# Optimization experiments

Hardware: AMD Instinct MI355X
Metric: run time of the kernel (lower is better)

The kernel has to match this reference:

```python
import jax, jax.numpy as jnp
import numpy as np

IN, HID, RANK, B = 2048, 2048, 512, 8192


def setup_inputs() -> dict:
    key = jax.random.key(0)
    ks = jax.random.split(key, 16)
    s_in = 1.0 / np.sqrt(IN + HID)
    s_r = 1.0 / np.sqrt(RANK)
    inp = {
        "x": jax.random.normal(ks[0], (B, IN), jnp.float32),
        "h": jax.random.normal(ks[1], (B, HID), jnp.float32),
        "c": jax.random.normal(ks[2], (B, HID), jnp.float32),
    }
    names = ["i", "f", "c", "o"]
    for idx, g in enumerate(names):
        inp[f"U{g}"] = jax.random.uniform(ks[3 + 3 * idx], (IN + HID, RANK), jnp.float32, -s_in, s_in)
        inp[f"V{g}"] = jax.random.uniform(ks[4 + 3 * idx], (RANK, HID), jnp.float32, -s_r, s_r)
        inp[f"b{g}"] = jnp.zeros((HID,), jnp.float32)
    return inp


def reference(x, h, c, Ui, Vi, bi, Uf, Vf, bf, Uc, Vc, bc, Uo, Vo, bo):
    combined = jnp.concatenate([x, h], axis=1)  # [B, IN+HID]

    def gate(U, V, b):
        return (combined @ U) @ V + b  # low-rank: [B,R] then [B,HID]

    i = jax.nn.sigmoid(gate(Ui, Vi, bi))
    f = jax.nn.sigmoid(gate(Uf, Vf, bf))
    o = jax.nn.sigmoid(gate(Uo, Vo, bo))
    c_hat = jnp.tanh(gate(Uc, Vc, bc))
    c_new = f * c + i * c_hat
    h_new = o * jnp.tanh(c_new)
    return (h_new, c_new)
```

## Files before the change

kernel.cpp:

```cpp
#include <hip/hip_runtime.h>
#include <hip/hip_bf16.h>
#include <cstdint>
#include <cstddef>

typedef __bf16 bf16;
typedef __bf16 bf16x8 __attribute__((ext_vector_type(8)));
typedef float f32x4 __attribute__((ext_vector_type(4)));

#define BATCH 8192
#define IN_DIM 2048
#define HID 2048
#define RANK 512
#define KDIM 4096
#define NG 2048
#define CHUNK_ROWS 4096


__device__ __forceinline__ void gload16(const void* g, void* l) {
  __builtin_amdgcn_global_load_lds(
      (const __attribute__((address_space(1))) unsigned int*)g,
      (__attribute__((address_space(3))) unsigned int*)l, 16, 0, 0);
}

__device__ __forceinline__ float sigmoidf_(float x) {
  return 1.0f / (1.0f + __expf(-x));
}
__device__ __forceinline__ float tanhf_(float x) {
  return 1.0f - 2.0f / (__expf(2.0f * x) + 1.0f);
}

__device__ __forceinline__ void stage_half(const bf16* __restrict__ g0, int ld,
                                           int row0, int kcol, bf16* lbase, int tid) {
  const int wid = tid >> 6;
  #pragma unroll
  for (int q = 0; q < 2; ++q) {
    const int slot = q * 512 + tid;
    const int row = slot >> 3, cb = slot & 7;
    const int gcb = cb ^ (row & 7);
    gload16(g0 + (size_t)(row0 + row) * ld + kcol + gcb * 8,
            lbase + (size_t)(q * 64 + wid * 8) * 64);
  }
}

#define GBAR  __builtin_amdgcn_s_barrier()
#define LGKM0 asm volatile("s_waitcnt lgkmcnt(0)" ::: "memory")
#define VMC4  asm volatile("s_waitcnt vmcnt(4)" ::: "memory")
#define VMC8  asm volatile("s_waitcnt vmcnt(8)" ::: "memory")
#define SB0   __builtin_amdgcn_sched_barrier(0)

#define LD_Ap(PA, Q)                                                          \
  _Pragma("unroll") for (int ai = 0; ai < 2; ++ai)                            \
  _Pragma("unroll") for (int ks = 0; ks < 2; ++ks)                            \
    a[ai][ks] = *(const bf16x8*)((PA) + (wm + (Q) * 32 + ai * 16 + lr) * 64   \
                                 + ((((ks << 2) | lk) ^ sw) << 3));

#define LD_Bp(PB)                                                             \
  _Pragma("unroll") for (int j = 0; j < 4; ++j)                               \
  _Pragma("unroll") for (int ks = 0; ks < 2; ++ks)                            \
    b[j][ks] = *(const bf16x8*)((PB) + (wn + j * 16 + lr) * 64                \
                                 + ((((ks << 2) | lk) ^ sw) << 3));

#define MFMAQ(Q)                                                              \
  _Pragma("unroll") for (int ai = 0; ai < 2; ++ai)                            \
  _Pragma("unroll") for (int ks = 0; ks < 2; ++ks)                            \
  _Pragma("unroll") for (int j = 0; j < 4; ++j)                               \
    acc[(Q) * 2 + ai][j] = __builtin_amdgcn_mfma_f32_16x16x32_bf16(           \
        a[ai][ks], b[j][ks], acc[(Q) * 2 + ai][j], 0, 0, 0);

#define PHASE3(TOP, STAGE, Q, PFOP, TAILVM) \
  {                                         \
    TOP;                                    \
    STAGE;                                  \
    GBAR;                                   \
    LGKM0;                                  \
    __builtin_amdgcn_s_setprio(1);          \
    MFMAQ(Q);                               \
    __builtin_amdgcn_s_setprio(0);          \
    PFOP;                                   \
    SB0;                                    \
    TAILVM;                                 \
    GBAR;                                   \
  }

template <int NT>
__device__ __forceinline__ void gemm_core(const bf16* __restrict__ A, int lda, int m0,
                                          const bf16* __restrict__ B, int ldb, int n0,
                                          bf16* lds, f32x4 (&acc)[8][4]) {
  const int tid = threadIdx.x;
  const int wid = tid >> 6, lane = tid & 63;
  const int wm = (wid >> 2) * 128, wn = (wid & 3) * 64;
  const int lr = lane & 15, lk = lane >> 4;
  const int sw = lr & 7;
  bf16x8 a[2][2], b[4][2];

  bf16* Ab0 = lds;
  bf16* Ab1 = lds + 16384;
  bf16* Rg0 = lds + 2 * 16384;
  bf16* Rg1 = lds + 3 * 16384;
  bf16* Rg2 = lds + 4 * 16384;

  #pragma unroll
  for (int i = 0; i < 8; ++i)
    #pragma unroll
    for (int j = 0; j < 4; ++j) acc[i][j] = (f32x4){0.f, 0.f, 0.f, 0.f};

  stage_half(A, lda, m0,       0,   Ab0,        tid);
  stage_half(A, lda, m0 + 128, 0,   Ab0 + 8192, tid);
  stage_half(B, ldb, n0,       0,   Rg0,        tid);
  stage_half(B, ldb, n0 + 128, 0,   Rg0 + 8192, tid);
  stage_half(B, ldb, n0,       64,  Rg1,        tid);
  stage_half(B, ldb, n0 + 128, 64,  Rg1 + 8192, tid);
  stage_half(B, ldb, n0,       128, Rg2,        tid);
  stage_half(B, ldb, n0 + 128, 128, Rg2 + 8192, tid);
  VMC8;
  GBAR;
  LD_Bp(Rg0);

  bf16 *pBc = Rg0, *pBn = Rg1, *pBn2 = Rg2;
  bf16 *pAc = Ab0, *pAa = Ab1;
  for (int c = 0; c < NT; ++c) {
    const int kc1 = ((c + 1) & (NT - 1)) * 64;
    const int kc3 = ((c + 3) & (NT - 1)) * 64;
    PHASE3(LD_Ap(pAc, 0), stage_half(A, lda, m0,       kc1, pAa,        tid), 0,
           LD_Ap(pAc, 1), (void)0);
    PHASE3((void)0,       stage_half(A, lda, m0 + 128, kc1, pAa + 8192, tid), 1,
           LD_Ap(pAc, 2), (void)0);
    PHASE3((void)0,       stage_half(B, ldb, n0,       kc3, pBc,        tid), 2,
           LD_Ap(pAc, 3), (void)0);
    PHASE3((void)0,       stage_half(B, ldb, n0 + 128, kc3, pBc + 8192, tid), 3,
           LD_Bp(pBn),    VMC4);
    bf16* tt = pBc; pBc = pBn; pBn = pBn2; pBn2 = tt;
    tt = pAc; pAc = pAa; pAa = tt;
  }
}


__global__ void k_convert_combined(const float* __restrict__ x,
                                   const float* __restrict__ h,
                                   bf16* __restrict__ out) {
  size_t i4 = (size_t)blockIdx.x * blockDim.x + threadIdx.x;
  size_t base = i4 * 4;
  int col = (int)(base & (KDIM - 1));
  size_t row = base >> 12;
  const float* src = (col < IN_DIM) ? (x + row * IN_DIM + col)
                                    : (h + row * (size_t)HID + (col - IN_DIM));
  float4 v = *(const float4*)src;
  union { bf16 b[4]; uint2 u; } p;
  p.b[0] = (bf16)v.x; p.b[1] = (bf16)v.y; p.b[2] = (bf16)v.z; p.b[3] = (bf16)v.w;
  *(uint2*)(out + base) = p.u;
}


__global__ void k_tconv4(const float* __restrict__ s0, const float* __restrict__ s1,
                         const float* __restrict__ s2, const float* __restrict__ s3,
                         bf16* __restrict__ out, int nrow, int ncol,
                         long ostride, long gstride) {
  __shared__ float t[32][33];
  const float* in = blockIdx.z == 0 ? s0 : blockIdx.z == 1 ? s1
                  : blockIdx.z == 2 ? s2 : s3;
  bf16* o = out + (size_t)blockIdx.z * gstride;
  int c0 = blockIdx.x * 32, r0 = blockIdx.y * 32;
  int tx = threadIdx.x, ty = threadIdx.y;
  #pragma unroll
  for (int yy = ty; yy < 32; yy += 8)
    t[yy][tx] = in[(size_t)(r0 + yy) * ncol + c0 + tx];
  __syncthreads();
  #pragma unroll
  for (int yy = ty; yy < 32; yy += 8)
    o[(size_t)(c0 + yy) * ostride + r0 + tx] = (bf16)t[tx][yy];
}


__launch_bounds__(512, 2)
__global__ void k_gemm1(const bf16* __restrict__ A,
                        const bf16* __restrict__ Bt,
                        bf16* __restrict__ R) {
  __shared__ __align__(16) bf16 lds[81920];
  const int bx = blockIdx.x;
  const int id = (bx & 7) * 32 + (bx >> 3);
  const int m0 = (id >> 3) * 256, n0 = (id & 7) * 256;
  f32x4 acc[8][4];
  gemm_core<KDIM / 64>(A, KDIM, m0, Bt, KDIM, n0, lds, acc);

  const int tid = threadIdx.x;
  const int wid = tid >> 6, lane = tid & 63;
  const int wm = (wid >> 2) * 128, wn = (wid & 3) * 64;
  const int lr = lane & 15, lk = lane >> 4;
  #pragma unroll
  for (int i = 0; i < 8; ++i)
    #pragma unroll
    for (int j = 0; j < 4; ++j)
      #pragma unroll
      for (int v = 0; v < 4; ++v)
        R[(size_t)(m0 + wm + i * 16 + lk * 4 + v) * NG + (n0 + wn + j * 16 + lr)] =
            (bf16)acc[i][j][v];
}


__launch_bounds__(512, 2)
__global__ void k_gates(const bf16* __restrict__ Rb,
                        const bf16* __restrict__ Vt,
                        const float* __restrict__ b0, const float* __restrict__ b1,
                        const float* __restrict__ b2, const float* __restrict__ b3,
                        bf16* __restrict__ G, int m_base) {
  __shared__ __align__(16) bf16 lds[81920];
  const int bx = blockIdx.x;
  const int id = (bx & 7) * 64 + (bx >> 3);
  const int gate = id >> 7;
  const int mo = ((id >> 3) & 15) * 256;
  const int n0 = (id & 7) * 256;
  f32x4 acc[8][4];
  gemm_core<RANK / 64>(Rb + gate * RANK, NG, m_base + mo,
                       Vt + (size_t)gate * HID * RANK, RANK, n0, lds, acc);

  const int tid = threadIdx.x;
  const int wid = tid >> 6, lane = tid & 63;
  const int wm = (wid >> 2) * 128, wn = (wid & 3) * 64;
  const int lr = lane & 15, lk = lane >> 4;
  const float* bias = gate == 0 ? b0 : gate == 1 ? b1 : gate == 2 ? b2 : b3;
  const bool is_tanh = (gate == 2);
  bf16* Gg = G + (size_t)gate * CHUNK_ROWS * HID;
  #pragma unroll
  for (int j = 0; j < 4; ++j) {
    const int col = n0 + wn + j * 16 + lr;
    const float bj = bias[col];
    #pragma unroll
    for (int i = 0; i < 8; ++i)
      #pragma unroll
      for (int v = 0; v < 4; ++v) {
        const int row = mo + wm + i * 16 + lk * 4 + v;
        float p = acc[i][j][v] + bj;
        float av = is_tanh ? tanhf_(p) : sigmoidf_(p);
        Gg[(size_t)row * HID + col] = (bf16)av;
      }
  }
}


__global__ void k_ew(const bf16* __restrict__ G,
                     const float* __restrict__ cin,
                     float* __restrict__ hout, float* __restrict__ cout,
                     int m_base) {
  const size_t CHUNK = (size_t)CHUNK_ROWS * HID;
  const bf16* Gi = G;
  const bf16* Gf = G + CHUNK;
  const bf16* Gc = G + 2 * CHUNK;
  const bf16* Go = G + 3 * CHUNK;
  const size_t n8 = CHUNK / 8;
  for (size_t t = (size_t)blockIdx.x * blockDim.x + threadIdx.x; t < n8;
       t += (size_t)gridDim.x * blockDim.x) {
    size_t e = t * 8;
    bf16x8 vi = *(const bf16x8*)(Gi + e);
    bf16x8 vf = *(const bf16x8*)(Gf + e);
    bf16x8 vc = *(const bf16x8*)(Gc + e);
    bf16x8 vo = *(const bf16x8*)(Go + e);
    size_t ge = (size_t)m_base * HID + e;
    float4 c0 = *(const float4*)(cin + ge);
    float4 c1 = *(const float4*)(cin + ge + 4);
    float cc[8] = {c0.x, c0.y, c0.z, c0.w, c1.x, c1.y, c1.z, c1.w};
    float cn[8], hn[8];
    #pragma unroll
    for (int v = 0; v < 8; ++v) {
      float iv = (float)vi[v], fv = (float)vf[v], cv = (float)vc[v], ov = (float)vo[v];
      cn[v] = fv * cc[v] + iv * cv;
      hn[v] = ov * tanhf_(cn[v]);
    }
    *(float4*)(cout + ge)     = (float4){cn[0], cn[1], cn[2], cn[3]};
    *(float4*)(cout + ge + 4) = (float4){cn[4], cn[5], cn[6], cn[7]};
    *(float4*)(hout + ge)     = (float4){hn[0], hn[1], hn[2], hn[3]};
    *(float4*)(hout + ge + 4) = (float4){hn[4], hn[5], hn[6], hn[7]};
  }
}


extern "C" void kernel_launch(void* const* d_in, const int* in_sizes, int n_in,
                              void* d_out, int out_size, void* d_ws, size_t ws_size,
                              hipStream_t stream) {
  const float* x = (const float*)d_in[0];
  const float* h = (const float*)d_in[1];
  const float* c = (const float*)d_in[2];
  const float* U[4] = {(const float*)d_in[3], (const float*)d_in[6],
                       (const float*)d_in[9], (const float*)d_in[12]};
  const float* V[4] = {(const float*)d_in[4], (const float*)d_in[7],
                       (const float*)d_in[10], (const float*)d_in[13]};
  const float* b[4] = {(const float*)d_in[5], (const float*)d_in[8],
                       (const float*)d_in[11], (const float*)d_in[14]};

  char* ws = (char*)d_ws;
  bf16* combined = (bf16*)ws;
  bf16* Ut       = (bf16*)(ws + 67108864);
  bf16* Vt       = (bf16*)(ws + 67108864 + 16777216);
  bf16* Rbuf     = (bf16*)(ws + 67108864 + 16777216 + 8388608);
  bf16* G        = (bf16*)ws;

  float* hout = (float*)d_out;
  float* cout = hout + (size_t)BATCH * HID;

  k_convert_combined<<<(BATCH * (size_t)KDIM / 4) / 256, 256, 0, stream>>>(x, h, combined);

  k_tconv4<<<dim3(RANK / 32, KDIM / 32, 4), dim3(32, 8), 0, stream>>>(
      U[0], U[1], U[2], U[3], Ut, KDIM, RANK, KDIM, (long)RANK * KDIM);
  k_tconv4<<<dim3(HID / 32, RANK / 32, 4), dim3(32, 8), 0, stream>>>(
      V[0], V[1], V[2], V[3], Vt, RANK, HID, RANK, (long)HID * RANK);

  k_gemm1<<<256, 512, 0, stream>>>(combined, Ut, Rbuf);

  for (int chunk = 0; chunk < 2; ++chunk) {
    int m_base = chunk * CHUNK_ROWS;
    k_gates<<<512, 512, 0, stream>>>(Rbuf, Vt, b[0], b[1], b[2], b[3], G, m_base);
    k_ew<<<2048, 256, 0, stream>>>(G, c, hout, cout, m_base);
  }
}
```

Baseline: 346.7 us.

## Fuse four gate GEMMs with LSTM elementwise update in one kernel

Replaces the chunked gate GEMM plus elementwise kernels with a single kernel in which each block computes all four gate GEMMs for its output tile in sequence. Gate results are combined in registers (i*c_hat, then the c update, then h), so the bf16 gate intermediates are never written to or read back from global memory, and launches drop from four to one. In exchange, grid size falls from 512 to 256 blocks, register pressure rises from the extra 128-float state array, and the cin/cout/hout accesses become strided scalar loads and stores from the MFMA layout instead of vectorized ones.

```diff
diff --git a/kernel.cpp b/kernel.cpp
--- a/kernel.cpp
+++ b/kernel.cpp
@@ -13,7 +13,6 @@
 #define RANK 512
 #define KDIM 4096
 #define NG 2048
-#define CHUNK_ROWS 4096
 
 
 __device__ __forceinline__ void gload16(const void* g, void* l) {
@@ -44,6 +43,7 @@
 
 #define GBAR  __builtin_amdgcn_s_barrier()
 #define LGKM0 asm volatile("s_waitcnt lgkmcnt(0)" ::: "memory")
+#define VMC0  asm volatile("s_waitcnt vmcnt(0)" ::: "memory")
 #define VMC4  asm volatile("s_waitcnt vmcnt(4)" ::: "memory")
 #define VMC8  asm volatile("s_waitcnt vmcnt(8)" ::: "memory")
 #define SB0   __builtin_amdgcn_sched_barrier(0)
@@ -198,77 +198,58 @@
 
 
 __launch_bounds__(512, 2)
-__global__ void k_gates(const bf16* __restrict__ Rb,
+__global__ void k_fused(const bf16* __restrict__ Rb,
                         const bf16* __restrict__ Vt,
-                        const float* __restrict__ b0, const float* __restrict__ b1,
-                        const float* __restrict__ b2, const float* __restrict__ b3,
-                        bf16* __restrict__ G, int m_base) {
+                        const float* __restrict__ bi, const float* __restrict__ bf_,
+                        const float* __restrict__ bc, const float* __restrict__ bo,
+                        const float* __restrict__ cin,
+                        float* __restrict__ hout, float* __restrict__ cout) {
   __shared__ __align__(16) bf16 lds[81920];
   const int bx = blockIdx.x;
-  const int id = (bx & 7) * 64 + (bx >> 3);
-  const int gate = id >> 7;
-  const int mo = ((id >> 3) & 15) * 256;
-  const int n0 = (id & 7) * 256;
-  f32x4 acc[8][4];
-  gemm_core<RANK / 64>(Rb + gate * RANK, NG, m_base + mo,
-                       Vt + (size_t)gate * HID * RANK, RANK, n0, lds, acc);
-
+  const int id = (bx & 7) * 32 + (bx >> 3);
+  const int m0 = (id >> 3) * 256, n0 = (id & 7) * 256;
   const int tid = threadIdx.x;
   const int wid = tid >> 6, lane = tid & 63;
   const int wm = (wid >> 2) * 128, wn = (wid & 3) * 64;
   const int lr = lane & 15, lk = lane >> 4;
-  const float* bias = gate == 0 ? b0 : gate == 1 ? b1 : gate == 2 ? b2 : b3;
-  const bool is_tanh = (gate == 2);
-  bf16* Gg = G + (size_t)gate * CHUNK_ROWS * HID;
-  #pragma unroll
-  for (int j = 0; j < 4; ++j) {
-    const int col = n0 + wn + j * 16 + lr;
-    const float bj = bias[col];
+
+  f32x4 acc[8][4];
+  float sv[8][4][4];
+
+  #pragma unroll 1
+  for (int gi = 0; gi < 4; ++gi) {
+    const int g = ((gi & 1) << 1) | (gi >> 1);
+    if (gi) {
+      VMC0;
+      GBAR;
+    }
+    gemm_core<RANK / 64>(Rb + g * RANK, NG, m0,
+                         Vt + (size_t)g * HID * RANK, RANK, n0, lds, acc);
+    const float* bias = g == 0 ? bi : g == 1 ? bf_ : g == 2 ? bc : bo;
     #pragma unroll
-    for (int i = 0; i < 8; ++i)
+    for (int j = 0; j < 4; ++j) {
+      const int col = n0 + wn + j * 16 + lr;
+      const float bj = bias[col];
       #pragma unroll
-      for (int v = 0; v < 4; ++v) {
-        const int row = mo + wm + i * 16 + lk * 4 + v;
-        float p = acc[i][j][v] + bj;
-        float av = is_tanh ? tanhf_(p) : sigmoidf_(p);
-        Gg[(size_t)row * HID + col] = (bf16)av;
-      }
-  }
-}
-
-
-__global__ void k_ew(const bf16* __restrict__ G,
-                     const float* __restrict__ cin,
-                     float* __restrict__ hout, float* __restrict__ cout,
-                     int m_base) {
-  const size_t CHUNK = (size_t)CHUNK_ROWS * HID;
-  const bf16* Gi = G;
-  const bf16* Gf = G + CHUNK;
-  const bf16* Gc = G + 2 * CHUNK;
-  const bf16* Go = G + 3 * CHUNK;
-  const size_t n8 = CHUNK / 8;
-  for (size_t t = (size_t)blockIdx.x * blockDim.x + threadIdx.x; t < n8;
-       t += (size_t)gridDim.x * blockDim.x) {
-    size_t e = t * 8;
-    bf16x8 vi = *(const bf16x8*)(Gi + e);
-    bf16x8 vf = *(const bf16x8*)(Gf + e);
-    bf16x8 vc = *(const bf16x8*)(Gc + e);
-    bf16x8 vo = *(const bf16x8*)(Go + e);
-    size_t ge = (size_t)m_base * HID + e;
-    float4 c0 = *(const float4*)(cin + ge);
-    float4 c1 = *(const float4*)(cin + ge + 4);
-    float cc[8] = {c0.x, c0.y, c0.z, c0.w, c1.x, c1.y, c1.z, c1.w};
-    float cn[8], hn[8];
-    #pragma unroll
-    for (int v = 0; v < 8; ++v) {
-      float iv = (float)vi[v], fv = (float)vf[v], cv = (float)vc[v], ov = (float)vo[v];
-      cn[v] = fv * cc[v] + iv * cv;
-      hn[v] = ov * tanhf_(cn[v]);
+      for (int i = 0; i < 8; ++i)
+        #pragma unroll
+        for (int v = 0; v < 4; ++v) {
+          const float p = acc[i][j][v] + bj;
+          if (gi == 0) {
+            sv[i][j][v] = sigmoidf_(p);
+          } else if (gi == 1) {
+            sv[i][j][v] *= tanhf_(p);
+          } else if (gi == 2) {
+            const int row = m0 + wm + i * 16 + lk * 4 + v;
+            const float cn = sigmoidf_(p) * cin[(size_t)row * HID + col] + sv[i][j][v];
+            cout[(size_t)row * HID + col] = cn;
+            sv[i][j][v] = tanhf_(cn);
+          } else {
+            const int row = m0 + wm + i * 16 + lk * 4 + v;
+            hout[(size_t)row * HID + col] = sigmoidf_(p) * sv[i][j][v];
+          }
+        }
     }
-    *(float4*)(cout + ge)     = (float4){cn[0], cn[1], cn[2], cn[3]};
-    *(float4*)(cout + ge + 4) = (float4){cn[4], cn[5], cn[6], cn[7]};
-    *(float4*)(hout + ge)     = (float4){hn[0], hn[1], hn[2], hn[3]};
-    *(float4*)(hout + ge + 4) = (float4){hn[4], hn[5], hn[6], hn[7]};
   }
 }
 
@@ -291,7 +272,6 @@
   bf16* Ut       = (bf16*)(ws + 67108864);
   bf16* Vt       = (bf16*)(ws + 67108864 + 16777216);
   bf16* Rbuf     = (bf16*)(ws + 67108864 + 16777216 + 8388608);
-  bf16* G        = (bf16*)ws;
 
   float* hout = (float*)d_out;
   float* cout = hout + (size_t)BATCH * HID;
@@ -305,9 +285,5 @@
 
   k_gemm1<<<256, 512, 0, stream>>>(combined, Ut, Rbuf);
 
-  for (int chunk = 0; chunk < 2; ++chunk) {
-    int m_base = chunk * CHUNK_ROWS;
-    k_gates<<<512, 512, 0, stream>>>(Rbuf, Vt, b[0], b[1], b[2], b[3], G, m_base);
-    k_ew<<<2048, 256, 0, stream>>>(G, c, hout, cout, m_base);
-  }
-}
+  k_fused<<<256, 512, 0, stream>>>(Rbuf, Vt, b[0], b[1], b[2], b[3], c, hout, cout);
+}
```

Result: slower. 639.3 us (+84.4%).

## Double-buffer A fragments in registers and use partial LDS waits in GEMM loop

Applied to the files above, without the earlier changes.

The GEMM main loop now keeps two register sets of A fragments, so the LDS reads for the next quarter-tile are issued before the MFMAs of the current one. The full lgkmcnt(0) wait becomes lgkmcnt(4), and the trailing barrier of each phase is dropped. The aim is to hide LDS read latency behind matrix math and cut barrier stalls. In exchange it uses more VGPRs and relies on the hand-set wait counts and remaining barriers to keep LDS reuse safe.

```diff
diff --git a/kernel.cpp b/kernel.cpp
--- a/kernel.cpp
+++ b/kernel.cpp
@@ -29,6 +29,12 @@
   return 1.0f - 2.0f / (__expf(2.0f * x) + 1.0f);
 }
 
+#define GBAR  __builtin_amdgcn_s_barrier()
+#define VMC4  asm volatile("s_waitcnt vmcnt(4)" ::: "memory")
+#define VMC8  asm volatile("s_waitcnt vmcnt(8)" ::: "memory")
+#define SB0   __builtin_amdgcn_sched_barrier(0)
+#define LGKMC(N) do { asm volatile("s_waitcnt lgkmcnt(" #N ")" ::: "memory"); SB0; } while (0)
+
 __device__ __forceinline__ void stage_half(const bf16* __restrict__ g0, int ld,
                                            int row0, int kcol, bf16* lbase, int tid) {
   const int wid = tid >> 6;
@@ -42,45 +48,25 @@
   }
 }
 
-#define GBAR  __builtin_amdgcn_s_barrier()
-#define LGKM0 asm volatile("s_waitcnt lgkmcnt(0)" ::: "memory")
-#define VMC4  asm volatile("s_waitcnt vmcnt(4)" ::: "memory")
-#define VMC8  asm volatile("s_waitcnt vmcnt(8)" ::: "memory")
-#define SB0   __builtin_amdgcn_sched_barrier(0)
-
-#define LD_Ap(PA, Q)                                                          \
-  _Pragma("unroll") for (int ai = 0; ai < 2; ++ai)                            \
-  _Pragma("unroll") for (int ks = 0; ks < 2; ++ks)                            \
-    a[ai][ks] = *(const bf16x8*)((PA) + (wm + (Q) * 32 + ai * 16 + lr) * 64   \
+#define LD_APAR(PA, Q, P)                                                      \
+  _Pragma("unroll") for (int ai = 0; ai < 2; ++ai)                             \
+  _Pragma("unroll") for (int ks = 0; ks < 2; ++ks)                             \
+    a[P][ai][ks] = *(const bf16x8*)((PA) + (wm + (Q) * 32 + ai * 16 + lr) * 64 \
                                  + ((((ks << 2) | lk) ^ sw) << 3));
 
-#define LD_Bp(PB)                                                             \
-  _Pragma("unroll") for (int j = 0; j < 4; ++j)                               \
-  _Pragma("unroll") for (int ks = 0; ks < 2; ++ks)                            \
-    b[j][ks] = *(const bf16x8*)((PB) + (wn + j * 16 + lr) * 64                \
+#define LD_Bp(PB)                                                              \
+  _Pragma("unroll") for (int j = 0; j < 4; ++j)                                \
+  _Pragma("unroll") for (int ks = 0; ks < 2; ++ks)                             \
+    b[j][ks] = *(const bf16x8*)((PB) + (wn + j * 16 + lr) * 64                 \
                                  + ((((ks << 2) | lk) ^ sw) << 3));
 
-#define MFMAQ(Q)                                                              \
-  _Pragma("unroll") for (int ai = 0; ai < 2; ++ai)                            \
-  _Pragma("unroll") for (int ks = 0; ks < 2; ++ks)                            \
-  _Pragma("unroll") for (int j = 0; j < 4; ++j)                               \
-    acc[(Q) * 2 + ai][j] = __builtin_amdgcn_mfma_f32_16x16x32_bf16(           \
-        a[ai][ks], b[j][ks], acc[(Q) * 2 + ai][j], 0, 0, 0);
-
-#define PHASE3(TOP, STAGE, Q, PFOP, TAILVM) \
-  {                                         \
-    TOP;                                    \
-    STAGE;                                  \
-    GBAR;                                   \
-    LGKM0;                                  \
-    __builtin_amdgcn_s_setprio(1);          \
-    MFMAQ(Q);                               \
-    __builtin_amdgcn_s_setprio(0);          \
-    PFOP;                                   \
-    SB0;                                    \
-    TAILVM;                                 \
-    GBAR;                                   \
-  }
+#define MFMAQP(Q, P)                                                           \
+  _Pragma("unroll") for (int ai = 0; ai < 2; ++ai)                             \
+  _Pragma("unroll") for (int ks = 0; ks < 2; ++ks)                             \
+  _Pragma("unroll") for (int j = 0; j < 4; ++j)                                \
+    acc[(Q) * 2 + ai][j] = __builtin_amdgcn_mfma_f32_16x16x32_bf16(            \
+        a[P][ai][ks], b[j][ks], acc[(Q) * 2 + ai][j], 0, 0, 0);
+
 
 template <int NT>
 __device__ __forceinline__ void gemm_core(const bf16* __restrict__ A, int lda, int m0,
@@ -91,7 +77,8 @@
   const int wm = (wid >> 2) * 128, wn = (wid & 3) * 64;
   const int lr = lane & 15, lk = lane >> 4;
   const int sw = lr & 7;
-  bf16x8 a[2][2], b[4][2];
+  bf16x8 a[2][2][2];
+  bf16x8 b[4][2];
 
   bf16* Ab0 = lds;
   bf16* Ab1 = lds + 16384;
@@ -115,20 +102,35 @@
   VMC8;
   GBAR;
   LD_Bp(Rg0);
+  SB0;
 
   bf16 *pBc = Rg0, *pBn = Rg1, *pBn2 = Rg2;
   bf16 *pAc = Ab0, *pAa = Ab1;
   for (int c = 0; c < NT; ++c) {
     const int kc1 = ((c + 1) & (NT - 1)) * 64;
     const int kc3 = ((c + 3) & (NT - 1)) * 64;
-    PHASE3(LD_Ap(pAc, 0), stage_half(A, lda, m0,       kc1, pAa,        tid), 0,
-           LD_Ap(pAc, 1), (void)0);
-    PHASE3((void)0,       stage_half(A, lda, m0 + 128, kc1, pAa + 8192, tid), 1,
-           LD_Ap(pAc, 2), (void)0);
-    PHASE3((void)0,       stage_half(B, ldb, n0,       kc3, pBc,        tid), 2,
-           LD_Ap(pAc, 3), (void)0);
-    PHASE3((void)0,       stage_half(B, ldb, n0 + 128, kc3, pBc + 8192, tid), 3,
-           LD_Bp(pBn),    VMC4);
+    LD_APAR(pAc, 0, 0); LD_APAR(pAc, 1, 1); SB0;
+    stage_half(A, lda, m0,       kc1, pAa,        tid); SB0;
+    GBAR;
+    LGKMC(4);
+    __builtin_amdgcn_s_setprio(1); MFMAQP(0, 0); __builtin_amdgcn_s_setprio(0);
+    LD_APAR(pAc, 2, 0); SB0;
+    stage_half(A, lda, m0 + 128, kc1, pAa + 8192, tid); SB0;
+    GBAR;
+    LGKMC(4);
+    __builtin_amdgcn_s_setprio(1); MFMAQP(1, 1); __builtin_amdgcn_s_setprio(0);
+    LD_APAR(pAc, 3, 1); SB0;
+    stage_half(B, ldb, n0,       kc3, pBc,        tid); SB0;
+    GBAR;
+    LGKMC(4);
+    __builtin_amdgcn_s_setprio(1); MFMAQP(2, 0); __builtin_amdgcn_s_setprio(0);
+    stage_half(B, ldb, n0 + 128, kc3, pBc + 8192, tid); SB0;
+    VMC4;
+    GBAR;
+    LGKMC(0);
+    __builtin_amdgcn_s_setprio(1); MFMAQP(3, 1); __builtin_amdgcn_s_setprio(0);
+    LD_Bp(pBn);
+    SB0;
     bf16* tt = pBc; pBc = pBn; pBn = pBn2; pBn2 = tt;
     tt = pAc; pAc = pAa; pAa = tt;
   }
```

After: 343.6 us. Within noise of the previous version (-0.9%).
